# Kernel optimization log

Hardware: AMD Instinct MI355X
Metric: run time of the kernel (lower is better)

Reference implementation:

```python
import jax, jax.numpy as jnp
import numpy as np
from jax import lax

EPS = 1e-5


def _dcn_core(value, offset, mask, offset_scale):
    # value: (B,H,W,G,D); offset: (B,H,W,G,K,2) as (dx,dy); mask: (B,H,W,G,K)
    # DCNv4: no softmax on mask; sampling loc = center + (kernel_grid + offset)*offset_scale
    B, H, W, G, D = value.shape
    K = mask.shape[-1]
    P = H * W
    kr = jnp.arange(3, dtype=value.dtype) - 1.0
    gy, gx = jnp.meshgrid(kr, kr, indexing="ij")  # 3x3 kernel grid
    gx = gx.reshape(1, 1, 1, 1, K)
    gy = gy.reshape(1, 1, 1, 1, K)
    bx = jnp.arange(W, dtype=value.dtype).reshape(1, 1, W, 1, 1)
    by = jnp.arange(H, dtype=value.dtype).reshape(1, H, 1, 1, 1)
    ix = bx + (gx + offset[..., 0]) * offset_scale  # (B,H,W,G,K) pixel-index coords
    iy = by + (gy + offset[..., 1]) * offset_scale

    tog = lambda a: a.transpose(0, 3, 1, 2, 4).reshape(B, G, P, K)
    ix, iy, m = tog(ix), tog(iy), tog(mask)
    vflat = value.transpose(0, 3, 1, 2, 4).reshape(B, G, P, D)

    x0 = jnp.floor(ix)
    y0 = jnp.floor(iy)
    tx = ix - x0
    ty = iy - y0
    out = jnp.zeros((B, G, P, D), value.dtype)
    # bilinear with zero padding (grid_sample padding_mode='zeros', align_corners=False)
    for dy, dx, wgt in ((0, 0, (1 - ty) * (1 - tx)), (0, 1, (1 - ty) * tx),
                        (1, 0, ty * (1 - tx)), (1, 1, ty * tx)):
        xc = x0 + dx
        yc = y0 + dy
        valid = ((xc >= 0) & (xc < W) & (yc >= 0) & (yc < H)).astype(value.dtype)
        lin = (jnp.clip(yc, 0, H - 1) * W + jnp.clip(xc, 0, W - 1)).astype(jnp.int32)
        v = jnp.take_along_axis(vflat, lin.reshape(B, G, P * K, 1), axis=2)
        v = v.reshape(B, G, P, K, D)
        out = out + jnp.einsum("bgpk,bgpkd->bgpd", wgt * m * valid, v)
    return out.transpose(0, 2, 1, 3).reshape(B, P, G * D)


def setup_inputs() -> dict:
    key = jax.random.key(0)
    ks = jax.random.split(key, 6)
    C = 64
    r = lambda k, shp, s: jax.random.normal(k, shp, jnp.float32) * s
    return {
        "x": r(ks[0], (8, C, 128, 128), 1.0),
        "vp_w": r(ks[1], (C, C), C ** -0.5),
        "vp_b": jnp.zeros((C,), jnp.float32),
        "dw_w": r(ks[2], (C, 1, 3, 3), 1.0 / 3.0),
        "dw_b": jnp.zeros((C,), jnp.float32),
        "om_w": r(ks[3], (56, C), 0.01),
        "om_b": jnp.zeros((56,), jnp.float32),
        "op_w": r(ks[4], (C, C), C ** -0.5),
        "op_b": jnp.zeros((C,), jnp.float32),
        "bn_g": jnp.ones((C // 2,), jnp.float32),
        "bn_b": jnp.zeros((C // 2,), jnp.float32),
        "bn_m": jnp.zeros((C // 2,), jnp.float32),
        "bn_v": jnp.ones((C // 2,), jnp.float32),
    }


def reference(x, vp_w, vp_b, dw_w, dw_b, om_w, om_b, op_w, op_b, bn_g, bn_b, bn_m, bn_v):
    B, C, H, W = x.shape
    G, K, OS = 2, 9, 2.0  # group = in_planes//out_planes = 2; 3x3 -> K=9
    seq = x.reshape(B, H * W, C)  # raw reshape exactly as the torch code
    # DCNv4 value_proj
    val = seq @ vp_w.T + vp_b
    value = val.reshape(B, H, W, G, C // G)
    # offset/mask branch: depthwise 3x3 conv on raw input, then linear
    xi = seq.reshape(B, H, W, C).transpose(0, 3, 1, 2)  # (B,C,H,W)
    dw = lax.conv_general_dilated(xi, dw_w, (1, 1), "SAME",
                                  dimension_numbers=("NCHW", "OIHW", "NCHW"),
                                  feature_group_count=C)
    dw = dw + dw_b[None, :, None, None]
    om = dw.transpose(0, 2, 3, 1) @ om_w.T + om_b  # (B,H,W,56)
    om = om[..., : G * K * 3].reshape(B, H, W, G, 3 * K)  # drop pad-to-8 tail
    offset = om[..., : 2 * K].reshape(B, H, W, G, K, 2)
    mask = om[..., 2 * K:]
    core = _dcn_core(value, offset, mask, OS)  # (B, HW, C)
    out = (core @ op_w.T + op_b).reshape(B, C, H, W)  # raw reshape, as in torch code
    z = 0.5 * (out[:, : C // 2] + out[:, C // 2:])  # chunk + average
    z = bn_g[:, None, None] * (z - bn_m[:, None, None]) * lax.rsqrt(bn_v + EPS)[:, None, None] + bn_b[:, None, None]
    return jnp.maximum(z, 0.0)
```

## Files before the change

### kernel.cpp

```cpp
#include <hip/hip_runtime.h>

#define B_ 8
#define H_ 128
#define W_ 128
#define P_ 16384
#define C_ 64
#define NQ (B_*P_)

typedef _Float16 fp16;
typedef _Float16 half2v __attribute__((ext_vector_type(2)));
typedef _Float16 half4v __attribute__((ext_vector_type(4)));
typedef _Float16 half8v __attribute__((ext_vector_type(8)));

static __device__ __forceinline__ void fma4s(float4& a, float s, const float4& v) {
  a.x += s * v.x; a.y += s * v.y; a.z += s * v.z; a.w += s * v.w;
}
static __device__ __forceinline__ void fma4e(float4& a, const float4& u, const float4& v) {
  a.x += u.x * v.x; a.y += u.y * v.y; a.z += u.z * v.z; a.w += u.w * v.w;
}
static __device__ __forceinline__ float4 h2f(half4v h) {
  return make_float4((float)h.x, (float)h.y, (float)h.z, (float)h.w);
}
static __device__ __forceinline__ half4v f2h(float4 a) {
  half4v hv;
  hv.x = (fp16)a.x; hv.y = (fp16)a.y; hv.z = (fp16)a.z; hv.w = (fp16)a.w;
  return hv;
}

__global__ __launch_bounds__(256) void gemm_val_kernel(
    const float* __restrict__ X, const float* __restrict__ W,
    const float* __restrict__ bias, fp16* __restrict__ val) {
  __shared__ __align__(16) float Xs[128][68];
  __shared__ __align__(16) float Ws[64][68];
  int tid = threadIdx.x;
  int bid = blockIdx.x;
  int logical = (bid & 7) * 128 + (bid >> 3);
  size_t row0 = (size_t)logical * 128;

#pragma unroll
  for (int i0 = 0; i0 < 8192; i0 += 1024) {
    int i = i0 + tid * 4;
    int r = i >> 6, k = i & 63;
    *(float4*)&Xs[r][k] = *(const float4*)(X + row0 * 64 + i);
  }
#pragma unroll
  for (int i0 = 0; i0 < 4096; i0 += 1024) {
    int i = i0 + tid * 4;
    int c = i >> 6, k = i & 63;
    float4 wv = *(const float4*)(W + i);
    Ws[k][c] = wv.x; Ws[k + 1][c] = wv.y; Ws[k + 2][c] = wv.z; Ws[k + 3][c] = wv.w;
  }
  __syncthreads();

  int ty = tid >> 4, tx = tid & 15;
  int c0 = tx * 4;
  float4 b4 = *(const float4*)(bias + c0);
  float4 acc[8];
#pragma unroll
  for (int rr = 0; rr < 8; ++rr) acc[rr] = b4;
#pragma unroll 4
  for (int k0 = 0; k0 < 64; k0 += 4) {
    float4 w0 = *(const float4*)&Ws[k0][c0];
    float4 w1 = *(const float4*)&Ws[k0 + 1][c0];
    float4 w2 = *(const float4*)&Ws[k0 + 2][c0];
    float4 w3 = *(const float4*)&Ws[k0 + 3][c0];
#pragma unroll
    for (int rr = 0; rr < 8; ++rr) {
      float4 xv = *(const float4*)&Xs[ty + rr * 16][k0];
      fma4s(acc[rr], xv.x, w0); fma4s(acc[rr], xv.y, w1);
      fma4s(acc[rr], xv.z, w2); fma4s(acc[rr], xv.w, w3);
    }
  }
#pragma unroll
  for (int rr = 0; rr < 8; ++rr) {
    int r = ty + rr * 16;
    *(half4v*)(val + (row0 + r) * 64 + c0) = f2h(acc[rr]);
  }
}

__global__ __launch_bounds__(256, 4) void dwom_kernel(
    const float* __restrict__ X, const float* __restrict__ dw_w,
    const float* __restrict__ dw_b, const float* __restrict__ om_w,
    const float* __restrict__ om_b, fp16* __restrict__ OM) {
  __shared__ __align__(16) float dws[64][68];
  __shared__ __align__(16) fp16 omwT[64][60];
  __shared__ __align__(16) float dwwT[9][68];
  __shared__ float dwbs[64];
  __shared__ float ombs[56];
  int tid = threadIdx.x;
  int bid = blockIdx.x;
  int logical = (bid & 7) * 256 + (bid >> 3);
  int b = logical >> 8;
  int lg = logical & 255;
  int q0 = b * 16384 + lg * 64;
  int h = lg >> 1;
  int w0 = (lg & 1) * 64;

  for (int i = tid; i < 3456; i += 256) omwT[i & 63][i >> 6] = (fp16)om_w[i];
  for (int i = tid; i < 576; i += 256) dwwT[i % 9][i / 9] = dw_w[i];
  if (tid < 64) dwbs[tid] = dw_b[tid];
  if (tid < 56) ombs[tid] = (tid < 54) ? om_b[tid] : 0.f;
  __syncthreads();

  {
    int cv = tid & 15;
    int wq = tid >> 4;
    int c0 = cv * 4;
    int wbase = w0 + wq * 4;
    const float* xb = X + (size_t)b * 1048576 + c0;
    bool v0 = (h > 0), v2 = (h < 127);
    const float4 z4 = make_float4(0.f, 0.f, 0.f, 0.f);
    float4 ra[3][6];
#pragma unroll
    for (int j = 0; j < 6; ++j) {
      int w = wbase + j - 1;
      bool vw = (unsigned)w < 128u;
      const float* base = xb + (size_t)w * 64;
      ra[0][j] = (vw && v0) ? *(const float4*)(base + (size_t)(h - 1) * 8192) : z4;
      ra[1][j] = vw         ? *(const float4*)(base + (size_t)h * 8192)       : z4;
      ra[2][j] = (vw && v2) ? *(const float4*)(base + (size_t)(h + 1) * 8192) : z4;
    }
    float4 dwb4 = *(const float4*)&dwbs[c0];
    float4 acc[4] = {dwb4, dwb4, dwb4, dwb4};
#pragma unroll
    for (int t = 0; t < 9; ++t) {
      float4 w = *(const float4*)&dwwT[t][c0];
      int r = t / 3, cb = t % 3;
#pragma unroll
      for (int j = 0; j < 4; ++j)
        fma4e(acc[j], ra[r][j + cb], w);
    }
#pragma unroll
    for (int j = 0; j < 4; ++j)
      *(float4*)&dws[wq * 4 + j][c0] = acc[j];
  }
  __syncthreads();

  int ty = tid >> 4, tx = tid & 15;
  int o0 = tx * 4;
  if (o0 < 54) {
    float4 b4 = *(const float4*)&ombs[o0];
    float4 acc[4] = {b4, b4, b4, b4};
#pragma unroll 4
    for (int k0 = 0; k0 < 64; k0 += 4) {
      float4 w0 = h2f(*(const half4v*)&omwT[k0][o0]);
      float4 w1 = h2f(*(const half4v*)&omwT[k0 + 1][o0]);
      float4 w2 = h2f(*(const half4v*)&omwT[k0 + 2][o0]);
      float4 w3 = h2f(*(const half4v*)&omwT[k0 + 3][o0]);
#pragma unroll
      for (int rr = 0; rr < 4; ++rr) {
        float4 dv = *(const float4*)&dws[ty * 4 + rr][k0];
        fma4s(acc[rr], dv.x, w0); fma4s(acc[rr], dv.y, w1);
        fma4s(acc[rr], dv.z, w2); fma4s(acc[rr], dv.w, w3);
      }
    }
#pragma unroll
    for (int rr = 0; rr < 4; ++rr) {
      int r = ty * 4 + rr;
      size_t base = (size_t)(q0 + r) * 54 + o0;
      if (o0 <= 48) {
        *(half4v*)(OM + base) = f2h(acc[rr]);
      } else {
        half2v hv2;
        hv2.x = (fp16)acc[rr].x; hv2.y = (fp16)acc[rr].y;
        *(half2v*)(OM + base) = hv2;
      }
    }
  }
}

__global__ __launch_bounds__(256, 4) void gather_kernel(
    const fp16* __restrict__ val, const fp16* __restrict__ OM,
    fp16* __restrict__ core) {
  __shared__ __align__(16) float4 wtab[64 * 2 * 9];
  __shared__ int btab[64 * 2 * 9];
  int tid = threadIdx.x;
  int bid = blockIdx.x;
  int logical = (bid & 7) * 256 + (bid >> 3);
  int b = logical >> 8;
  int q0 = logical * 64;

  for (int i = tid; i < 1152; i += 256) {
    int row = i / 18;
    int rem = i - row * 18;
    int g = rem / 9;
    int k = rem - g * 9;
    int q = q0 + row;
    int p = q & 16383;
    int h = p >> 7, w = p & 127;
    const fp16* omq = OM + (size_t)q * 54 + g * 27;
    float ox = (float)omq[2 * k], oy = (float)omq[2 * k + 1];
    float m = (float)omq[18 + k];
    int kx = k - (k / 3) * 3, ky = k / 3;
    float ix = (float)w + ((float)kx - 1.0f + ox) * 2.0f;
    float iy = (float)h + ((float)ky - 1.0f + oy) * 2.0f;
    float x0f = floorf(ix), y0f = floorf(iy);
    float tx = ix - x0f, ty = iy - y0f;
    int x0 = (int)x0f, y0 = (int)y0f;
    int x1 = x0 + 1, y1 = y0 + 1;
    float vx0 = ((unsigned)x0 < 128u) ? 1.f : 0.f;
    float vx1 = ((unsigned)x1 < 128u) ? 1.f : 0.f;
    float vy0 = ((unsigned)y0 < 128u) ? 1.f : 0.f;
    float vy1 = ((unsigned)y1 < 128u) ? 1.f : 0.f;
    int xc0 = min(max(x0, 0), 127), xc1 = min(max(x1, 0), 127);
    int yc0 = min(max(y0, 0), 127), yc1 = min(max(y1, 0), 127);
    float4 w4;
    w4.x = (1.f - ty) * (1.f - tx) * m * vy0 * vx0;
    w4.y = (1.f - ty) * tx * m * vy0 * vx1;
    w4.z = ty * (1.f - tx) * m * vy1 * vx0;
    w4.w = ty * tx * m * vy1 * vx1;
    wtab[i] = w4;
    btab[i] = (yc0 * 128 + xc0) | ((xc1 - xc0) << 14) | ((yc1 - yc0) << 15);
  }
  __syncthreads();

  int lq = tid >> 4;
  int g = (tid >> 3) & 1;
  int dv = tid & 7;
  const fp16* vbase = val + ((size_t)b << 20) + g * 32 + dv * 4;
  fp16* cbase = core + (size_t)q0 * 64 + g * 32 + dv * 4;
  for (int t = 0; t < 4; ++t) {
    int row = lq + 16 * t;
    int base = (row * 2 + g) * 9;
    float4 acc = make_float4(0.f, 0.f, 0.f, 0.f);
#pragma unroll
    for (int k = 0; k < 9; ++k) {
      float4 w4 = wtab[base + k];
      int pk = btab[base + k];
      int lin00 = pk & 16383;
      int dxo = (pk >> 14) & 1;
      int lin10 = lin00 + ((pk >> 15) << 7);
      half4v v00 = *(const half4v*)(vbase + ((size_t)lin00 << 6));
      half4v v01 = *(const half4v*)(vbase + ((size_t)(lin00 + dxo) << 6));
      half4v v10 = *(const half4v*)(vbase + ((size_t)lin10 << 6));
      half4v v11 = *(const half4v*)(vbase + ((size_t)(lin10 + dxo) << 6));
      fma4s(acc, w4.x, h2f(v00));
      fma4s(acc, w4.y, h2f(v01));
      fma4s(acc, w4.z, h2f(v10));
      fma4s(acc, w4.w, h2f(v11));
    }
    *(half4v*)(cbase + ((size_t)row << 6)) = f2h(acc);
  }
}

__global__ __launch_bounds__(256) void gemmbn_kernel(
    const fp16* __restrict__ core, const float* __restrict__ op_w,
    const float* __restrict__ op_b, const float* __restrict__ bn_g,
    const float* __restrict__ bn_b, const float* __restrict__ bn_m,
    const float* __restrict__ bn_v, float* __restrict__ out) {
  __shared__ __align__(16) float Ws[64][68];
  __shared__ __align__(16) fp16 csL[64][72];
  __shared__ __align__(16) fp16 csH[64][72];
  int tid = threadIdx.x;
  int bid = blockIdx.x;
  int logical = (bid & 7) * 128 + (bid >> 3);
  int b = logical >> 7;
  int p0 = (logical & 127) * 64;
  size_t q0lo = (size_t)b * 16384 + p0;

#pragma unroll
  for (int i0 = 0; i0 < 4096; i0 += 1024) {
    int i = i0 + tid * 4;
    int c = i >> 6, k = i & 63;
    float4 wv = *(const float4*)(op_w + i);
    Ws[k][c] = wv.x; Ws[k + 1][c] = wv.y; Ws[k + 2][c] = wv.z; Ws[k + 3][c] = wv.w;
  }
#pragma unroll
  for (int j0 = 0; j0 < 512; j0 += 256) {
    int j = j0 + tid;
    int r = j >> 3;
    int cc = (j & 7) * 8;
    *(half8v*)&csL[r][cc] = *(const half8v*)(core + (q0lo + r) * 64 + cc);
    *(half8v*)&csH[r][cc] = *(const half8v*)(core + (q0lo + 8192 + r) * 64 + cc);
  }
  __syncthreads();

  int ty = tid >> 4, tx = tid & 15;
  int c0 = tx * 4;
  float4 accL[4], accH[4];
#pragma unroll
  for (int m = 0; m < 4; ++m) {
    accL[m] = make_float4(0.f, 0.f, 0.f, 0.f);
    accH[m] = make_float4(0.f, 0.f, 0.f, 0.f);
  }
#pragma unroll 2
  for (int k0 = 0; k0 < 64; k0 += 4) {
    float4 w0 = *(const float4*)&Ws[k0][c0];
    float4 w1 = *(const float4*)&Ws[k0 + 1][c0];
    float4 w2 = *(const float4*)&Ws[k0 + 2][c0];
    float4 w3 = *(const float4*)&Ws[k0 + 3][c0];
#pragma unroll
    for (int m = 0; m < 4; ++m) {
      int r = ty + 16 * m;
      float4 aL = h2f(*(const half4v*)&csL[r][k0]);
      float4 aH = h2f(*(const half4v*)&csH[r][k0]);
      fma4s(accL[m], aL.x, w0); fma4s(accL[m], aL.y, w1);
      fma4s(accL[m], aL.z, w2); fma4s(accL[m], aL.w, w3);
      fma4s(accH[m], aH.x, w0); fma4s(accH[m], aH.y, w1);
      fma4s(accH[m], aH.z, w2); fma4s(accH[m], aH.w, w3);
    }
  }
  float4 bias4 = *(const float4*)(op_b + c0);
#pragma unroll
  for (int m = 0; m < 4; ++m) {
    int r = ty + 16 * m;
    int f = (p0 + r) * 64 + c0;
    int c2 = f >> 14;
    float scale = bn_g[c2] * rsqrtf(bn_v[c2] + 1e-5f);
    float shift = bn_b[c2] - bn_m[c2] * scale;
    float4 z;
    z.x = fmaxf((0.5f * (accL[m].x + accH[m].x) + bias4.x) * scale + shift, 0.f);
    z.y = fmaxf((0.5f * (accL[m].y + accH[m].y) + bias4.y) * scale + shift, 0.f);
    z.z = fmaxf((0.5f * (accL[m].z + accH[m].z) + bias4.z) * scale + shift, 0.f);
    z.w = fmaxf((0.5f * (accL[m].w + accH[m].w) + bias4.w) * scale + shift, 0.f);
    *(float4*)(out + (size_t)b * 524288 + f) = z;
  }
}

extern "C" void kernel_launch(void* const* d_in, const int* in_sizes, int n_in,
                              void* d_out, int out_size, void* d_ws, size_t ws_size,
                              hipStream_t stream) {
  const float* x    = (const float*)d_in[0];
  const float* vp_w = (const float*)d_in[1];
  const float* vp_b = (const float*)d_in[2];
  const float* dw_w = (const float*)d_in[3];
  const float* dw_b = (const float*)d_in[4];
  const float* om_w = (const float*)d_in[5];
  const float* om_b = (const float*)d_in[6];
  const float* op_w = (const float*)d_in[7];
  const float* op_b = (const float*)d_in[8];
  const float* bn_g = (const float*)d_in[9];
  const float* bn_b = (const float*)d_in[10];
  const float* bn_m = (const float*)d_in[11];
  const float* bn_v = (const float*)d_in[12];

  fp16* val_h  = (fp16*)d_ws;
  fp16* core_h = (fp16*)((char*)d_ws + (16u << 20));
  fp16* om_h   = (fp16*)((char*)d_ws + (32u << 20));

  gemm_val_kernel<<<dim3(1024), dim3(256), 0, stream>>>(x, vp_w, vp_b, val_h);
  dwom_kernel<<<dim3(2048), dim3(256), 0, stream>>>(x, dw_w, dw_b, om_w, om_b, om_h);
  gather_kernel<<<dim3(2048), dim3(256), 0, stream>>>(val_h, om_h, core_h);
  gemmbn_kernel<<<dim3(1024), dim3(256), 0, stream>>>(
      core_h, op_w, op_b, bn_g, bn_b, bn_m, bn_v, (float*)d_out);
}
```

Measured before the change: 125.3 us.

## Fuse value projection GEMM into depthwise conv/offset kernel reusing loaded input

Drops the separate value-projection GEMM kernel and computes it inside the depthwise-conv/offset-mask kernel, reusing the center-row input tile the conv already loads (stored as fp16 in shared memory). This saves one kernel launch and a second full read of the 32 MB input. In exchange the fused kernel uses more shared memory and registers (launch bounds lowered to 3 blocks), rounds the input and weights to fp16 before the projection, and each block redundantly reloads vp_w. The gather kernel's launch bounds are also raised to 6 blocks for occupancy.

```diff
diff --git a/kernel.cpp b/kernel.cpp
--- a/kernel.cpp
+++ b/kernel.cpp
@@ -27,63 +27,16 @@
   return hv;
 }
 
-__global__ __launch_bounds__(256) void gemm_val_kernel(
-    const float* __restrict__ X, const float* __restrict__ W,
-    const float* __restrict__ bias, fp16* __restrict__ val) {
-  __shared__ __align__(16) float Xs[128][68];
-  __shared__ __align__(16) float Ws[64][68];
-  int tid = threadIdx.x;
-  int bid = blockIdx.x;
-  int logical = (bid & 7) * 128 + (bid >> 3);
-  size_t row0 = (size_t)logical * 128;
-
-#pragma unroll
-  for (int i0 = 0; i0 < 8192; i0 += 1024) {
-    int i = i0 + tid * 4;
-    int r = i >> 6, k = i & 63;
-    *(float4*)&Xs[r][k] = *(const float4*)(X + row0 * 64 + i);
-  }
-#pragma unroll
-  for (int i0 = 0; i0 < 4096; i0 += 1024) {
-    int i = i0 + tid * 4;
-    int c = i >> 6, k = i & 63;
-    float4 wv = *(const float4*)(W + i);
-    Ws[k][c] = wv.x; Ws[k + 1][c] = wv.y; Ws[k + 2][c] = wv.z; Ws[k + 3][c] = wv.w;
-  }
-  __syncthreads();
-
-  int ty = tid >> 4, tx = tid & 15;
-  int c0 = tx * 4;
-  float4 b4 = *(const float4*)(bias + c0);
-  float4 acc[8];
-#pragma unroll
-  for (int rr = 0; rr < 8; ++rr) acc[rr] = b4;
-#pragma unroll 4
-  for (int k0 = 0; k0 < 64; k0 += 4) {
-    float4 w0 = *(const float4*)&Ws[k0][c0];
-    float4 w1 = *(const float4*)&Ws[k0 + 1][c0];
-    float4 w2 = *(const float4*)&Ws[k0 + 2][c0];
-    float4 w3 = *(const float4*)&Ws[k0 + 3][c0];
-#pragma unroll
-    for (int rr = 0; rr < 8; ++rr) {
-      float4 xv = *(const float4*)&Xs[ty + rr * 16][k0];
-      fma4s(acc[rr], xv.x, w0); fma4s(acc[rr], xv.y, w1);
-      fma4s(acc[rr], xv.z, w2); fma4s(acc[rr], xv.w, w3);
-    }
-  }
-#pragma unroll
-  for (int rr = 0; rr < 8; ++rr) {
-    int r = ty + rr * 16;
-    *(half4v*)(val + (row0 + r) * 64 + c0) = f2h(acc[rr]);
-  }
-}
-
-__global__ __launch_bounds__(256, 4) void dwom_kernel(
-    const float* __restrict__ X, const float* __restrict__ dw_w,
+__global__ __launch_bounds__(256, 3) void dwomval_kernel(
+    const float* __restrict__ X, const float* __restrict__ vp_w,
+    const float* __restrict__ vp_b, const float* __restrict__ dw_w,
     const float* __restrict__ dw_b, const float* __restrict__ om_w,
-    const float* __restrict__ om_b, fp16* __restrict__ OM) {
+    const float* __restrict__ om_b, fp16* __restrict__ val,
+    fp16* __restrict__ OM) {
+  __shared__ __align__(16) fp16 Ws[64][68];
+  __shared__ __align__(16) fp16 omwT[64][60];
+  __shared__ __align__(16) fp16 Xs[64][72];
   __shared__ __align__(16) float dws[64][68];
-  __shared__ __align__(16) fp16 omwT[64][60];
   __shared__ __align__(16) float dwwT[9][68];
   __shared__ float dwbs[64];
   __shared__ float ombs[56];
@@ -96,11 +49,11 @@
   int h = lg >> 1;
   int w0 = (lg & 1) * 64;
 
+  for (int i = tid; i < 4096; i += 256) Ws[i & 63][i >> 6] = (fp16)vp_w[i];
   for (int i = tid; i < 3456; i += 256) omwT[i & 63][i >> 6] = (fp16)om_w[i];
   for (int i = tid; i < 576; i += 256) dwwT[i % 9][i / 9] = dw_w[i];
   if (tid < 64) dwbs[tid] = dw_b[tid];
   if (tid < 56) ombs[tid] = (tid < 54) ? om_b[tid] : 0.f;
-  __syncthreads();
 
   {
     int cv = tid & 15;
@@ -131,27 +84,53 @@
         fma4e(acc[j], ra[r][j + cb], w);
     }
 #pragma unroll
-    for (int j = 0; j < 4; ++j)
-      *(float4*)&dws[wq * 4 + j][c0] = acc[j];
+    for (int j = 0; j < 4; ++j) {
+      int lq = wq * 4 + j;
+      *(float4*)&dws[lq][c0] = acc[j];
+      *(half4v*)&Xs[lq][c0] = f2h(ra[1][j + 1]);
+    }
   }
   __syncthreads();
 
   int ty = tid >> 4, tx = tid & 15;
+  int c0 = tx * 4;
+
+  {
+    float4 b4 = *(const float4*)(vp_b + c0);
+    float4 acc[4] = {b4, b4, b4, b4};
+#pragma unroll 4
+    for (int k0 = 0; k0 < 64; k0 += 4) {
+      float4 w0v = h2f(*(const half4v*)&Ws[k0][c0]);
+      float4 w1v = h2f(*(const half4v*)&Ws[k0 + 1][c0]);
+      float4 w2v = h2f(*(const half4v*)&Ws[k0 + 2][c0]);
+      float4 w3v = h2f(*(const half4v*)&Ws[k0 + 3][c0]);
+#pragma unroll
+      for (int rr = 0; rr < 4; ++rr) {
+        float4 xv = h2f(*(const half4v*)&Xs[ty * 4 + rr][k0]);
+        fma4s(acc[rr], xv.x, w0v); fma4s(acc[rr], xv.y, w1v);
+        fma4s(acc[rr], xv.z, w2v); fma4s(acc[rr], xv.w, w3v);
+      }
+    }
+#pragma unroll
+    for (int rr = 0; rr < 4; ++rr)
+      *(half4v*)(val + (size_t)(q0 + ty * 4 + rr) * 64 + c0) = f2h(acc[rr]);
+  }
+
   int o0 = tx * 4;
   if (o0 < 54) {
     float4 b4 = *(const float4*)&ombs[o0];
     float4 acc[4] = {b4, b4, b4, b4};
 #pragma unroll 4
     for (int k0 = 0; k0 < 64; k0 += 4) {
-      float4 w0 = h2f(*(const half4v*)&omwT[k0][o0]);
-      float4 w1 = h2f(*(const half4v*)&omwT[k0 + 1][o0]);
-      float4 w2 = h2f(*(const half4v*)&omwT[k0 + 2][o0]);
-      float4 w3 = h2f(*(const half4v*)&omwT[k0 + 3][o0]);
+      float4 w0v = h2f(*(const half4v*)&omwT[k0][o0]);
+      float4 w1v = h2f(*(const half4v*)&omwT[k0 + 1][o0]);
+      float4 w2v = h2f(*(const half4v*)&omwT[k0 + 2][o0]);
+      float4 w3v = h2f(*(const half4v*)&omwT[k0 + 3][o0]);
 #pragma unroll
       for (int rr = 0; rr < 4; ++rr) {
         float4 dv = *(const float4*)&dws[ty * 4 + rr][k0];
-        fma4s(acc[rr], dv.x, w0); fma4s(acc[rr], dv.y, w1);
-        fma4s(acc[rr], dv.z, w2); fma4s(acc[rr], dv.w, w3);
+        fma4s(acc[rr], dv.x, w0v); fma4s(acc[rr], dv.y, w1v);
+        fma4s(acc[rr], dv.z, w2v); fma4s(acc[rr], dv.w, w3v);
       }
     }
 #pragma unroll
@@ -169,7 +148,7 @@
   }
 }
 
-__global__ __launch_bounds__(256, 4) void gather_kernel(
+__global__ __launch_bounds__(256, 6) void gather_kernel(
     const fp16* __restrict__ val, const fp16* __restrict__ OM,
     fp16* __restrict__ core) {
   __shared__ __align__(16) float4 wtab[64 * 2 * 9];
@@ -338,8 +317,8 @@
   fp16* core_h = (fp16*)((char*)d_ws + (16u << 20));
   fp16* om_h   = (fp16*)((char*)d_ws + (32u << 20));
 
-  gemm_val_kernel<<<dim3(1024), dim3(256), 0, stream>>>(x, vp_w, vp_b, val_h);
-  dwom_kernel<<<dim3(2048), dim3(256), 0, stream>>>(x, dw_w, dw_b, om_w, om_b, om_h);
+  dwomval_kernel<<<dim3(2048), dim3(256), 0, stream>>>(
+      x, vp_w, vp_b, dw_w, dw_b, om_w, om_b, val_h, om_h);
   gather_kernel<<<dim3(2048), dim3(256), 0, stream>>>(val_h, om_h, core_h);
   gemmbn_kernel<<<dim3(1024), dim3(256), 0, stream>>>(
       core_h, op_w, op_b, bn_g, bn_b, bn_m, bn_v, (float*)d_out);
```

New measurement: 124.4 us. No clear change (-0.8%).
